# Kernel optimization log

Hardware: AMD Instinct MI355X
Metric: run time of the kernel (lower is better)

## Reference

```python
import jax, jax.numpy as jnp
import numpy as np


def setup_inputs() -> dict:
    key = jax.random.key(0)
    ks = jax.random.split(key, 8)
    B, L, E, U = 32, 2048, 1024, 1024
    s = 0.02
    return {
        "dec_hidden": jax.random.normal(ks[0], (B, E), jnp.float32),
        "enc_output": jax.random.normal(ks[1], (B, L, E), jnp.float32),
        "prev_coverage": jax.random.uniform(ks[2], (B, L, 1), jnp.float32),
        "Ws_k": jax.random.normal(ks[3], (E, U), jnp.float32) * s,
        "Ws_b": jnp.zeros((U,), jnp.float32),
        "Wh_k": jax.random.normal(ks[4], (E, U), jnp.float32) * s,
        "Wh_b": jnp.zeros((U,), jnp.float32),
        "Wc_k": jax.random.normal(ks[5], (1, U), jnp.float32) * s,
        "Wc_b": jnp.zeros((U,), jnp.float32),
        "V_k": jax.random.normal(ks[6], (U, 1), jnp.float32) * s,
        "V_b": jnp.zeros((1,), jnp.float32),
        "enc_pad_mask": jnp.ones((B, L), jnp.int32),
        "use_coverage": 1,
    }


def reference(dec_hidden, enc_output, prev_coverage, Ws_k, Ws_b, Wh_k, Wh_b,
              Wc_k, Wc_b, V_k, V_b, enc_pad_mask, use_coverage):
    # projections: [B,L,U] + [B,1,U] (+ [B,L,U] coverage term)
    pre = jnp.einsum('ble,eu->blu', enc_output, Ws_k) + Ws_b \
        + (dec_hidden @ Wh_k + Wh_b)[:, None, :]
    if use_coverage:
        pre = pre + (prev_coverage @ Wc_k + Wc_b)
    score = jnp.tanh(pre) @ V_k + V_b              # [B, L, 1]
    mask = enc_pad_mask.astype(score.dtype)        # [B, L]
    masked_score = (score[..., 0] * mask)[..., None]  # [B, L, 1]
    attention_weights = jax.nn.softmax(masked_score, axis=1)
    coverage = attention_weights + prev_coverage if use_coverage else attention_weights
    context_vector = jnp.sum(attention_weights * enc_output, axis=1)  # [B, E]
    return (context_vector, attention_weights, coverage)
```

## Files before the change

kernel.cpp:

```cpp
#include <hip/hip_runtime.h>
#include <hip/hip_bf16.h>
#include <math.h>

typedef float f32x4 __attribute__((ext_vector_type(4)));
typedef short short8 __attribute__((ext_vector_type(8)));
typedef unsigned short u16x8 __attribute__((ext_vector_type(8)));

static __device__ __forceinline__ unsigned short f2bf(float f) {
    unsigned u = __builtin_bit_cast(unsigned, f);
    unsigned r = (u + 0x7FFFu + ((u >> 16) & 1u)) >> 16;
    return (unsigned short)r;
}
static __device__ __forceinline__ float bf2f(unsigned short h) {
    unsigned u = ((unsigned)h) << 16;
    return __builtin_bit_cast(float, u);
}
static __device__ __forceinline__ float fast_tanh(float x) {
    float ax = fminf(fmaxf(x, -9.f), 9.f);
    float e = __expf(2.f * ax);
    return 1.f - 2.f / (e + 1.f);
}

#define GLD16(g, l) __builtin_amdgcn_global_load_lds(                        \
    (const __attribute__((address_space(1))) void*)(g),                      \
    (__attribute__((address_space(3))) void*)(l), 16, 0, 0)

__global__ __launch_bounds__(256) void prep_kernel(
    const float* __restrict__ enc, unsigned short* __restrict__ encB,
    const float* __restrict__ ws, unsigned short* __restrict__ wst,
    const float* __restrict__ dh, const float* __restrict__ whk,
    float* __restrict__ base_part)
{
    __shared__ unsigned short tile[64][65];
    __shared__ float dS[128];
    const int bid = blockIdx.x, tid = threadIdx.x;

    if (bid < 16384) {
        const size_t base0 = (size_t)bid * 4096;
#pragma unroll
        for (int i = 0; i < 4; i++) {
            size_t g = base0 + (size_t)i * 1024 + tid * 4;
            f32x4 v = *(const f32x4*)(enc + g);
            ushort4 w;
            w.x = f2bf(v.x); w.y = f2bf(v.y); w.z = f2bf(v.z); w.w = f2bf(v.w);
            *(ushort4*)(encB + g) = w;
        }
    } else if (bid < 16640) {
        const int b2 = bid - 16384;
        const int e0 = (b2 & 15) * 64, u0 = (b2 >> 4) * 64;
#pragma unroll
        for (int i = 0; i < 16; i++) {
            int idx = i * 256 + tid;
            int r = idx >> 6, c = idx & 63;
            tile[r][c] = f2bf(ws[(size_t)(e0 + r) * 1024 + u0 + c]);
        }
        __syncthreads();
#pragma unroll
        for (int i = 0; i < 16; i++) {
            int idx = i * 256 + tid;
            int r = idx >> 6, c = idx & 63;
            wst[(size_t)(u0 + r) * 1024 + e0 + c] = tile[c][r];
        }
    } else {
        const int b3 = bid - 16640;
        const int b = b3 & 31, ec = b3 >> 5;
        const int e0 = ec * 128;
        if (tid < 128) dS[tid] = dh[b * 1024 + e0 + tid];
        __syncthreads();
        f32x4 acc = {0.f, 0.f, 0.f, 0.f};
#pragma unroll 4
        for (int e = 0; e < 128; e++)
            acc += dS[e] * *(const f32x4*)(whk + (size_t)(e0 + e) * 1024 + tid * 4);
        *(f32x4*)(base_part + (size_t)ec * 32768 + b * 1024 + tid * 4) = acc;
    }
}

#define BM 128
#define BN 128
#define BK 32

__global__ __launch_bounds__(256) void score_gemm_fast(
    const unsigned short* __restrict__ encB,
    const unsigned short* __restrict__ wst,
    const float* __restrict__ base_part,
    const float* __restrict__ cov,
    const float* __restrict__ wc,
    const float* __restrict__ vk,
    const float* __restrict__ wsb, const float* __restrict__ whb,
    const float* __restrict__ wcb,
    const int* __restrict__ ucov,
    float* __restrict__ score_part)
{
    __shared__ unsigned short As[2][BM * BK];
    __shared__ unsigned short Bs[2][BN * BK];
    __shared__ float covS[BM];
    __shared__ float baseS[BN], wcS[BN], vvS[BN];
    __shared__ float sred[2][BM];

    const int tid  = threadIdx.x;
    const int row0 = blockIdx.x * BM;
    const int u0   = blockIdx.y * BN;
    const int b    = row0 >> 11;
    const int use_cov = *ucov;

    if (tid < BM) covS[tid] = use_cov ? cov[row0 + tid] : 0.f;
    if (tid < BN) {
        int u = u0 + tid;
        float s = wsb[u] + whb[u] + (use_cov ? wcb[u] : 0.f);
#pragma unroll
        for (int p = 0; p < 8; p++) s += base_part[p * 32768 + b * 1024 + u];
        baseS[tid] = s;
        wcS[tid]   = use_cov ? wc[u] : 0.f;
        vvS[tid]   = vk[u];
    }

    const int lane = tid & 63;
    const int wid  = tid >> 6;
    const int wm   = wid >> 1, wn = wid & 1;
    const int l16  = lane & 15, quad = lane >> 4;

    const int f0 = tid, f1 = 256 + tid;
    const int rA0 = f0 >> 2, rA1 = f1 >> 2;
    const int cA0 = ((f0 & 3) - rA0 - (rA0 >> 2)) & 3;
    const int cA1 = ((f1 & 3) - rA1 - (rA1 >> 2)) & 3;
    const unsigned short* pA0 = encB + (size_t)(row0 + rA0) * 1024 + cA0 * 8;
    const unsigned short* pA1 = encB + (size_t)(row0 + rA1) * 1024 + cA1 * 8;
    const unsigned short* pB0 = wst + (size_t)(u0 + rA0) * 1024 + cA0 * 8;
    const unsigned short* pB1 = wst + (size_t)(u0 + rA1) * 1024 + cA1 * 8;

    int offA[4], offB[4];
#pragma unroll
    for (int t = 0; t < 4; t++) {
        int ra = wm * 64 + t * 16 + l16;
        offA[t] = (ra * 4 + ((quad + ra + (ra >> 2)) & 3)) * 8;
        int rb = wn * 64 + t * 16 + l16;
        offB[t] = (rb * 4 + ((quad + rb + (rb >> 2)) & 3)) * 8;
    }

    f32x4 acc[4][4] = {};

    GLD16(pA0, &As[0][f0 * 8]);
    GLD16(pA1, &As[0][f1 * 8]);
    GLD16(pB0, &Bs[0][f0 * 8]);
    GLD16(pB1, &Bs[0][f1 * 8]);
    pA0 += BK; pA1 += BK; pB0 += BK; pB1 += BK;
    __syncthreads();

    for (int kk = 0; kk < 32; kk++) {
        const int cur = kk & 1, nxt = cur ^ 1;
        if (kk < 31) {
            GLD16(pA0, &As[nxt][f0 * 8]);
            GLD16(pA1, &As[nxt][f1 * 8]);
            GLD16(pB0, &Bs[nxt][f0 * 8]);
            GLD16(pB1, &Bs[nxt][f1 * 8]);
            pA0 += BK; pA1 += BK; pB0 += BK; pB1 += BK;
        }
        short8 a[4], bb[4];
#pragma unroll
        for (int t = 0; t < 4; t++) {
            a[t]  = *(const short8*)&As[cur][offA[t]];
            bb[t] = *(const short8*)&Bs[cur][offB[t]];
        }
#pragma unroll
        for (int i = 0; i < 4; i++)
#pragma unroll
            for (int j = 0; j < 4; j++)
                acc[i][j] = __builtin_amdgcn_mfma_f32_16x16x32_bf16(a[i], bb[j], acc[i][j], 0, 0, 0);
        __syncthreads();
    }

#pragma unroll
    for (int i = 0; i < 4; i++) {
        float part[4] = {0.f, 0.f, 0.f, 0.f};
#pragma unroll
        for (int r = 0; r < 4; r++) {
            int rl = wm * 64 + i * 16 + quad * 4 + r;
            float cv = covS[rl];
#pragma unroll
            for (int j = 0; j < 4; j++) {
                int ul = wn * 64 + j * 16 + l16;
                float pre = acc[i][j][r] + baseS[ul] + cv * wcS[ul];
                part[r] += fast_tanh(pre) * vvS[ul];
            }
        }
#pragma unroll
        for (int r = 0; r < 4; r++) {
            float v = part[r];
            v += __shfl_xor(v, 1);
            v += __shfl_xor(v, 2);
            v += __shfl_xor(v, 4);
            v += __shfl_xor(v, 8);
            if (l16 == 0) sred[wn][wm * 64 + i * 16 + quad * 4 + r] = v;
        }
    }
    __syncthreads();
    if (tid < BM)
        score_part[(size_t)blockIdx.y * 65536 + row0 + tid] = sred[0][tid] + sred[1][tid];
}

__global__ __launch_bounds__(1024) void softmax_kernel(
    const float* __restrict__ score_part, int nplanes,
    const float* __restrict__ vb,
    const int* __restrict__ mask, const float* __restrict__ cov,
    const int* __restrict__ ucov,
    float* __restrict__ attn_out, float* __restrict__ cov_out)
{
    __shared__ float redA[16], redB[16];
    __shared__ float bc0, bc1;
    const int b = blockIdx.x, tid = threadIdx.x;
    const int i0 = b * 2048 + tid, i1 = i0 + 1024;
    const float vbv = vb[0];
    const int uc = *ucov;

    float s0 = 0.f, s1 = 0.f;
    for (int p = 0; p < nplanes; p++) {
        s0 += score_part[(size_t)p * 65536 + i0];
        s1 += score_part[(size_t)p * 65536 + i1];
    }
    s0 = (s0 + vbv) * (float)mask[i0];
    s1 = (s1 + vbv) * (float)mask[i1];

    float m = fmaxf(s0, s1);
#pragma unroll
    for (int off = 1; off < 64; off <<= 1) m = fmaxf(m, __shfl_xor(m, off));
    if ((tid & 63) == 0) redA[tid >> 6] = m;
    __syncthreads();
    if (tid < 16) {
        float v = redA[tid];
#pragma unroll
        for (int off = 1; off < 16; off <<= 1) v = fmaxf(v, __shfl_xor(v, off));
        if (tid == 0) bc0 = v;
    }
    __syncthreads();
    const float M = bc0;

    float e0 = __expf(s0 - M), e1 = __expf(s1 - M);
    float s = e0 + e1;
#pragma unroll
    for (int off = 1; off < 64; off <<= 1) s += __shfl_xor(s, off);
    if ((tid & 63) == 0) redB[tid >> 6] = s;
    __syncthreads();
    if (tid < 16) {
        float v = redB[tid];
#pragma unroll
        for (int off = 1; off < 16; off <<= 1) v += __shfl_xor(v, off);
        if (tid == 0) bc1 = v;
    }
    __syncthreads();
    const float inv = 1.f / bc1;

    float a0 = e0 * inv, a1 = e1 * inv;
    attn_out[i0] = a0;
    attn_out[i1] = a1;
    cov_out[i0] = a0 + (uc ? cov[i0] : 0.f);
    cov_out[i1] = a1 + (uc ? cov[i1] : 0.f);
}

__global__ __launch_bounds__(256) void context_bf16(const unsigned short* __restrict__ encB,
                                                    const float* __restrict__ attn,
                                                    float* __restrict__ out_ctx) {
    __shared__ float aS[2048];
    __shared__ float red[4][64];
    const int b = blockIdx.x, ec = blockIdx.y, tid = threadIdx.x;
    const int e0 = ec * 64;
    for (int i = tid; i < 2048; i += 256) aS[i] = attn[b * 2048 + i];
    __syncthreads();
    const int es = (tid & 7) * 8;
    const int lo = tid >> 3;
    float acc[8] = {};
    for (int l = lo; l < 2048; l += 32) {
        u16x8 w = *(const u16x8*)(encB + (size_t)(b * 2048 + l) * 1024 + e0 + es);
        float a = aS[l];
#pragma unroll
        for (int j = 0; j < 8; j++) acc[j] = fmaf(a, bf2f(w[j]), acc[j]);
    }
#pragma unroll
    for (int j = 0; j < 8; j++) {
        float v = acc[j];
        v += __shfl_xor(v, 8);
        v += __shfl_xor(v, 16);
        v += __shfl_xor(v, 32);
        acc[j] = v;
    }
    const int wv = tid >> 6;
    if ((tid & 63) < 8) {
#pragma unroll
        for (int j = 0; j < 8; j++) red[wv][(tid & 7) * 8 + j] = acc[j];
    }
    __syncthreads();
    if (tid < 64)
        out_ctx[b * 1024 + e0 + tid] = red[0][tid] + red[1][tid] + red[2][tid] + red[3][tid];
}

#define LDT 40
__global__ __launch_bounds__(256) void score_gemm_f32(
    const float* __restrict__ enc, const unsigned short* __restrict__ wst,
    const float* __restrict__ base_part, const float* __restrict__ cov,
    const float* __restrict__ wc, const float* __restrict__ vk,
    const float* __restrict__ wsb, const float* __restrict__ whb,
    const float* __restrict__ wcb,
    const int* __restrict__ ucov, float* __restrict__ score)
{
    __shared__ unsigned short As[BM * LDT];
    __shared__ unsigned short Bs[BN * LDT];
    __shared__ float covS[BM];
    __shared__ float baseS[BN], wcS[BN], vvS[BN];
    const int tid = threadIdx.x;
    const int row0 = blockIdx.x * BM, u0 = blockIdx.y * BN;
    const int b = row0 >> 11;
    const int use_cov = *ucov;
    if (tid < BM) covS[tid] = use_cov ? cov[row0 + tid] : 0.f;
    if (tid < BN) {
        int u = u0 + tid;
        float s = wsb[u] + whb[u] + (use_cov ? wcb[u] : 0.f);
#pragma unroll
        for (int p = 0; p < 8; p++) s += base_part[p * 32768 + b * 1024 + u];
        baseS[tid] = s;
        wcS[tid] = use_cov ? wc[u] : 0.f;
        vvS[tid] = vk[u];
    }
    const int lane = tid & 63, wid = tid >> 6;
    const int wm = wid >> 1, wn = wid & 1;
    const int l16 = lane & 15, quad = lane >> 4;
    f32x4 acc[4][4] = {};
    for (int k0 = 0; k0 < 1024; k0 += BK) {
        __syncthreads();
#pragma unroll
        for (int i = 0; i < 4; i++) {
            int f = i * 256 + tid;
            int r = f >> 3, c4 = f & 7;
            const float* p = enc + (size_t)(row0 + r) * 1024 + k0 + c4 * 4;
            ushort4 w;
            w.x = f2bf(p[0]); w.y = f2bf(p[1]); w.z = f2bf(p[2]); w.w = f2bf(p[3]);
            *(ushort4*)&As[r * LDT + c4 * 4] = w;
        }
#pragma unroll
        for (int i = 0; i < 2; i++) {
            int f = i * 256 + tid;
            int r = f >> 2, c8 = f & 3;
            uint4 w = *(const uint4*)(wst + (size_t)(u0 + r) * 1024 + k0 + c8 * 8);
            *(uint4*)&Bs[r * LDT + c8 * 8] = w;
        }
        __syncthreads();
        short8 a[4], bb[4];
#pragma unroll
        for (int t = 0; t < 4; t++) {
            a[t]  = *(const short8*)&As[(wm * 64 + t * 16 + l16) * LDT + quad * 8];
            bb[t] = *(const short8*)&Bs[(wn * 64 + t * 16 + l16) * LDT + quad * 8];
        }
#pragma unroll
        for (int i = 0; i < 4; i++)
#pragma unroll
            for (int j = 0; j < 4; j++)
                acc[i][j] = __builtin_amdgcn_mfma_f32_16x16x32_bf16(a[i], bb[j], acc[i][j], 0, 0, 0);
    }
#pragma unroll
    for (int i = 0; i < 4; i++) {
        float part[4] = {0.f, 0.f, 0.f, 0.f};
#pragma unroll
        for (int r = 0; r < 4; r++) {
            float cv = covS[wm * 64 + i * 16 + quad * 4 + r];
#pragma unroll
            for (int j = 0; j < 4; j++) {
                int ul = wn * 64 + j * 16 + l16;
                part[r] += fast_tanh(acc[i][j][r] + baseS[ul] + cv * wcS[ul]) * vvS[ul];
            }
        }
#pragma unroll
        for (int r = 0; r < 4; r++) {
            float v = part[r];
            v += __shfl_xor(v, 1);
            v += __shfl_xor(v, 2);
            v += __shfl_xor(v, 4);
            v += __shfl_xor(v, 8);
            if (l16 == 0)
                atomicAdd(&score[row0 + wm * 64 + i * 16 + quad * 4 + r], v);
        }
    }
}

__global__ __launch_bounds__(256) void context_f32(const float* __restrict__ enc,
                                                   const float* __restrict__ attn,
                                                   float* __restrict__ ctx) {
    __shared__ float aS[128];
    const int b = blockIdx.x, lc = blockIdx.y, tid = threadIdx.x;
    const int l0 = lc * 128;
    if (tid < 128) aS[tid] = attn[b * 2048 + l0 + tid];
    __syncthreads();
    const float* p = enc + ((size_t)(b * 2048 + l0)) * 1024 + tid * 4;
    f32x4 acc = {0.f, 0.f, 0.f, 0.f};
#pragma unroll 4
    for (int l = 0; l < 128; l++) acc += *(const f32x4*)(p + (size_t)l * 1024) * aS[l];
    float* o = ctx + b * 1024 + tid * 4;
    atomicAdd(o + 0, acc.x);
    atomicAdd(o + 1, acc.y);
    atomicAdd(o + 2, acc.z);
    atomicAdd(o + 3, acc.w);
}

__global__ __launch_bounds__(256) void prep2_kernel(
    const float* __restrict__ ws, unsigned short* __restrict__ wst,
    const float* __restrict__ dh, const float* __restrict__ whk,
    float* __restrict__ base_part)
{
    __shared__ unsigned short tile[64][65];
    __shared__ float dS[128];
    const int bid = blockIdx.x, tid = threadIdx.x;
    if (bid < 256) {
        const int e0 = (bid & 15) * 64, u0 = (bid >> 4) * 64;
#pragma unroll
        for (int i = 0; i < 16; i++) {
            int idx = i * 256 + tid;
            int r = idx >> 6, c = idx & 63;
            tile[r][c] = f2bf(ws[(size_t)(e0 + r) * 1024 + u0 + c]);
        }
        __syncthreads();
#pragma unroll
        for (int i = 0; i < 16; i++) {
            int idx = i * 256 + tid;
            int r = idx >> 6, c = idx & 63;
            wst[(size_t)(u0 + r) * 1024 + e0 + c] = tile[c][r];
        }
    } else {
        const int b3 = bid - 256;
        const int b = b3 & 31, ec = b3 >> 5;
        const int e0 = ec * 128;
        if (tid < 128) dS[tid] = dh[b * 1024 + e0 + tid];
        __syncthreads();
        f32x4 acc = {0.f, 0.f, 0.f, 0.f};
#pragma unroll 4
        for (int e = 0; e < 128; e++)
            acc += dS[e] * *(const f32x4*)(whk + (size_t)(e0 + e) * 1024 + tid * 4);
        *(f32x4*)(base_part + (size_t)ec * 32768 + b * 1024 + tid * 4) = acc;
    }
}

extern "C" void kernel_launch(void* const* d_in, const int* in_sizes, int n_in,
                              void* d_out, int out_size, void* d_ws, size_t ws_size,
                              hipStream_t stream) {
    const float* dec_hidden = (const float*)d_in[0];
    const float* enc        = (const float*)d_in[1];
    const float* prev_cov   = (const float*)d_in[2];
    const float* Ws_k       = (const float*)d_in[3];
    const float* Ws_b       = (const float*)d_in[4];
    const float* Wh_k       = (const float*)d_in[5];
    const float* Wh_b       = (const float*)d_in[6];
    const float* Wc_k       = (const float*)d_in[7];
    const float* Wc_b       = (const float*)d_in[8];
    const float* V_k        = (const float*)d_in[9];
    const float* V_b        = (const float*)d_in[10];
    const int*   mask       = (const int*)d_in[11];
    const int*   ucov       = (const int*)d_in[12];

    float* out_ctx  = (float*)d_out;
    float* out_attn = out_ctx + 32 * 1024;
    float* out_cov  = out_attn + 65536;

    char* ws = (char*)d_ws;
    unsigned short* wst = (unsigned short*)ws;
    float* base_part  = (float*)(ws + 2097152);
    float* score_part = (float*)(ws + 3145728);
    unsigned short* encB = (unsigned short*)(ws + 5242880);
    const size_t need_fast = 5242880 + (size_t)32 * 2048 * 1024 * 2;

    if (ws_size >= need_fast) {
        prep_kernel<<<16896, 256, 0, stream>>>(enc, encB, Ws_k, wst, dec_hidden, Wh_k, base_part);
        score_gemm_fast<<<dim3(512, 8), 256, 0, stream>>>(
            encB, wst, base_part, prev_cov, Wc_k, V_k, Ws_b, Wh_b, Wc_b, ucov, score_part);
        softmax_kernel<<<32, 1024, 0, stream>>>(score_part, 8, V_b, mask, prev_cov, ucov, out_attn, out_cov);
        context_bf16<<<dim3(32, 16), 256, 0, stream>>>(encB, out_attn, out_ctx);
    } else {
        hipMemsetAsync(score_part, 0, 65536 * sizeof(float), stream);
        hipMemsetAsync(out_ctx, 0, 32 * 1024 * sizeof(float), stream);
        prep2_kernel<<<512, 256, 0, stream>>>(Ws_k, wst, dec_hidden, Wh_k, base_part);
        score_gemm_f32<<<dim3(512, 8), 256, 0, stream>>>(
            enc, wst, base_part, prev_cov, Wc_k, V_k, Ws_b, Wh_b, Wc_b, ucov, score_part);
        softmax_kernel<<<32, 1024, 0, stream>>>(score_part, 1, V_b, mask, prev_cov, ucov, out_attn, out_cov);
        context_f32<<<dim3(32, 16), 256, 0, stream>>>(enc, out_attn, out_ctx);
    }
}
```

Measured before the change: 653.6 us.

## Replace score GEMM with 256x256 eight-phase pipelined MFMA kernel

Rewrites the bf16 score GEMM as 256x256 tiles with 512 threads, a K-step of 64 and an eight-phase schedule. Global-to-LDS loads are interleaved with MFMA groups using explicit barriers, vmcnt waits, sched_barriers and s_setprio. It also XOR-swizzles LDS, remaps blocks for locality, and cuts score partial planes from 8 to 4. The aim is more data reuse per tile and better overlap of memory with compute, at the cost of more registers and LDS, fewer resident blocks, and a fragile hand-tuned schedule.

```diff
diff --git a/kernel.cpp b/kernel.cpp
--- a/kernel.cpp
+++ b/kernel.cpp
@@ -75,11 +75,14 @@
     }
 }
 
-#define BM 128
-#define BN 128
-#define BK 32
-
-__global__ __launch_bounds__(256) void score_gemm_fast(
+#define SBAR()  __builtin_amdgcn_sched_barrier(0)
+#define BARR()  __builtin_amdgcn_s_barrier()
+#define PRIO1() __builtin_amdgcn_s_setprio(1)
+#define PRIO0() __builtin_amdgcn_s_setprio(0)
+#define VMC8()  asm volatile("s_waitcnt vmcnt(8)" ::: "memory")
+#define VMC0()  asm volatile("s_waitcnt vmcnt(0)" ::: "memory")
+
+__global__ __launch_bounds__(512, 2) void score_gemm_8ph(
     const unsigned short* __restrict__ encB,
     const unsigned short* __restrict__ wst,
     const float* __restrict__ base_part,
@@ -91,111 +94,201 @@
     const int* __restrict__ ucov,
     float* __restrict__ score_part)
 {
-    __shared__ unsigned short As[2][BM * BK];
-    __shared__ unsigned short Bs[2][BN * BK];
-    __shared__ float covS[BM];
-    __shared__ float baseS[BN], wcS[BN], vvS[BN];
-    __shared__ float sred[2][BM];
-
-    const int tid  = threadIdx.x;
-    const int row0 = blockIdx.x * BM;
-    const int u0   = blockIdx.y * BN;
-    const int b    = row0 >> 11;
-    const int use_cov = *ucov;
-
-    if (tid < BM) covS[tid] = use_cov ? cov[row0 + tid] : 0.f;
-    if (tid < BN) {
-        int u = u0 + tid;
-        float s = wsb[u] + whb[u] + (use_cov ? wcb[u] : 0.f);
-#pragma unroll
-        for (int p = 0; p < 8; p++) s += base_part[p * 32768 + b * 1024 + u];
-        baseS[tid] = s;
-        wcS[tid]   = use_cov ? wc[u] : 0.f;
-        vvS[tid]   = vk[u];
-    }
+    __shared__ __align__(16) unsigned short As[2][16384];
+    __shared__ __align__(16) unsigned short Bs[2][16384];
+
+    const int tid = threadIdx.x;
+    const int bid = blockIdx.x;
+    const int sidx = bid >> 3;
+    const int row_blk = (bid & 7) * 32 + (sidx >> 2);
+    const int u_blk = sidx & 3;
+    const int row0 = row_blk << 8;
+    const int u0 = u_blk << 8;
 
     const int lane = tid & 63;
     const int wid  = tid >> 6;
-    const int wm   = wid >> 1, wn = wid & 1;
-    const int l16  = lane & 15, quad = lane >> 4;
-
-    const int f0 = tid, f1 = 256 + tid;
-    const int rA0 = f0 >> 2, rA1 = f1 >> 2;
-    const int cA0 = ((f0 & 3) - rA0 - (rA0 >> 2)) & 3;
-    const int cA1 = ((f1 & 3) - rA1 - (rA1 >> 2)) & 3;
-    const unsigned short* pA0 = encB + (size_t)(row0 + rA0) * 1024 + cA0 * 8;
-    const unsigned short* pA1 = encB + (size_t)(row0 + rA1) * 1024 + cA1 * 8;
-    const unsigned short* pB0 = wst + (size_t)(u0 + rA0) * 1024 + cA0 * 8;
-    const unsigned short* pB1 = wst + (size_t)(u0 + rA1) * 1024 + cA1 * 8;
-
-    int offA[4], offB[4];
-#pragma unroll
-    for (int t = 0; t < 4; t++) {
-        int ra = wm * 64 + t * 16 + l16;
-        offA[t] = (ra * 4 + ((quad + ra + (ra >> 2)) & 3)) * 8;
-        int rb = wn * 64 + t * 16 + l16;
-        offB[t] = (rb * 4 + ((quad + rb + (rb >> 2)) & 3)) * 8;
-    }
-
-    f32x4 acc[4][4] = {};
-
-    GLD16(pA0, &As[0][f0 * 8]);
-    GLD16(pA1, &As[0][f1 * 8]);
-    GLD16(pB0, &Bs[0][f0 * 8]);
-    GLD16(pB1, &Bs[0][f1 * 8]);
-    pA0 += BK; pA1 += BK; pB0 += BK; pB1 += BK;
-    __syncthreads();
-
-    for (int kk = 0; kk < 32; kk++) {
-        const int cur = kk & 1, nxt = cur ^ 1;
-        if (kk < 31) {
-            GLD16(pA0, &As[nxt][f0 * 8]);
-            GLD16(pA1, &As[nxt][f1 * 8]);
-            GLD16(pB0, &Bs[nxt][f0 * 8]);
-            GLD16(pB1, &Bs[nxt][f1 * 8]);
-            pA0 += BK; pA1 += BK; pB0 += BK; pB1 += BK;
-        }
-        short8 a[4], bb[4];
-#pragma unroll
-        for (int t = 0; t < 4; t++) {
-            a[t]  = *(const short8*)&As[cur][offA[t]];
-            bb[t] = *(const short8*)&Bs[cur][offB[t]];
-        }
-#pragma unroll
-        for (int i = 0; i < 4; i++)
-#pragma unroll
-            for (int j = 0; j < 4; j++)
-                acc[i][j] = __builtin_amdgcn_mfma_f32_16x16x32_bf16(a[i], bb[j], acc[i][j], 0, 0, 0);
-        __syncthreads();
-    }
-
-#pragma unroll
-    for (int i = 0; i < 4; i++) {
+    const int wm = wid >> 2, wn = wid & 3;
+    const int l16 = lane & 15, quad = lane >> 4;
+
+    const int k8 = (lane & 7) ^ (lane >> 3);
+    unsigned offA[2][2], offB[2][2];
+    int dstA[2][2], dstB[2][2];
+#pragma unroll
+    for (int g = 0; g < 2; g++) {
+        const int uu = wid * 2 + g;
+#pragma unroll
+        for (int h = 0; h < 2; h++) {
+            const int ra = ((uu & 8) << 4) + (h << 6) + ((uu & 7) << 3);
+            const int rb = ((uu >> 2) << 6) + (h << 5) + ((uu & 3) << 3);
+            dstA[g][h] = ra * 64 + lane * 8;
+            dstB[g][h] = rb * 64 + lane * 8;
+            offA[g][h] = (unsigned)(row0 + ra + (lane >> 3)) * 1024u + (unsigned)(k8 * 8);
+            offB[g][h] = (unsigned)(u0 + rb + (lane >> 3)) * 1024u + (unsigned)(k8 * 8);
+        }
+    }
+
+    const int aBase = (wm * 128 + l16) * 64;
+    const int bBase = (wn * 64 + l16) * 64;
+    const int ch0 = ((quad) ^ (l16 & 7)) * 8;
+    const int ch1 = ((4 + quad) ^ (l16 & 7)) * 8;
+
+#define STAGE_A(bf, h, kt) do {                                             \
+    GLD16(encB + offA[0][h] + ((kt) << 6), &As[bf][dstA[0][h]]);            \
+    GLD16(encB + offA[1][h] + ((kt) << 6), &As[bf][dstA[1][h]]); } while (0)
+#define STAGE_B(bf, h, kt) do {                                             \
+    GLD16(wst + offB[0][h] + ((kt) << 6), &Bs[bf][dstB[0][h]]);             \
+    GLD16(wst + offB[1][h] + ((kt) << 6), &Bs[bf][dstB[1][h]]); } while (0)
+
+    f32x4 acc[8][4] = {};
+    short8 aF[4][2], bF0[2][2], bF1[2][2];
+
+#define LOAD_AF(bf, r) do {                                                 \
+    _Pragma("unroll")                                                       \
+    for (int fi = 0; fi < 4; fi++) {                                        \
+        aF[fi][0] = *(const short8*)&As[bf][aBase + (r)*4096 + fi*1024 + ch0]; \
+        aF[fi][1] = *(const short8*)&As[bf][aBase + (r)*4096 + fi*1024 + ch1]; \
+    } } while (0)
+#define LOAD_BF(bf, c, BF) do {                                             \
+    _Pragma("unroll")                                                       \
+    for (int fj = 0; fj < 2; fj++) {                                        \
+        BF[fj][0] = *(const short8*)&Bs[bf][bBase + (c)*2048 + fj*1024 + ch0]; \
+        BF[fj][1] = *(const short8*)&Bs[bf][bBase + (c)*2048 + fj*1024 + ch1]; \
+    } } while (0)
+#define MFMA16(r, c, BF) do {                                               \
+    _Pragma("unroll")                                                       \
+    for (int ks = 0; ks < 2; ks++)                                          \
+    _Pragma("unroll")                                                       \
+    for (int fi = 0; fi < 4; fi++)                                          \
+    _Pragma("unroll")                                                       \
+    for (int fj = 0; fj < 2; fj++)                                          \
+        acc[(r)*4+fi][(c)*2+fj] = __builtin_amdgcn_mfma_f32_16x16x32_bf16(  \
+            aF[fi][ks], BF[fj][ks], acc[(r)*4+fi][(c)*2+fj], 0, 0, 0);      \
+    } while (0)
+
+    STAGE_A(0, 0, 0);
+    STAGE_B(0, 0, 0);
+    STAGE_B(0, 1, 0);
+    STAGE_A(0, 1, 0);
+    STAGE_A(1, 0, 1);
+    STAGE_B(1, 0, 1);
+    STAGE_B(1, 1, 1);
+
+#pragma unroll 1
+    for (int i = 0; i < 7; i++) {
+        const int t1 = 2 * i + 1, t2 = 2 * i + 2, t3 = 2 * i + 3;
+        STAGE_A(1, 1, t1);
+        VMC8();
+        SBAR(); BARR(); SBAR();
+        LOAD_AF(0, 0); LOAD_BF(0, 0, bF0);
+        PRIO1(); MFMA16(0, 0, bF0); PRIO0();
+        SBAR(); BARR(); SBAR();
+        LOAD_BF(0, 1, bF1);
+        STAGE_A(0, 0, t2);
+        SBAR(); BARR(); SBAR();
+        PRIO1(); MFMA16(0, 1, bF1); PRIO0();
+        SBAR(); BARR(); SBAR();
+        LOAD_AF(0, 1);
+        STAGE_B(0, 0, t2);
+        SBAR(); BARR(); SBAR();
+        PRIO1(); MFMA16(1, 0, bF0); PRIO0();
+        SBAR(); BARR(); SBAR();
+        STAGE_B(0, 1, t2);
+        SBAR(); BARR(); SBAR();
+        PRIO1(); MFMA16(1, 1, bF1); PRIO0();
+        SBAR(); BARR(); SBAR();
+        STAGE_A(0, 1, t2);
+        VMC8();
+        SBAR(); BARR(); SBAR();
+        LOAD_AF(1, 0); LOAD_BF(1, 0, bF0);
+        PRIO1(); MFMA16(0, 0, bF0); PRIO0();
+        SBAR(); BARR(); SBAR();
+        LOAD_BF(1, 1, bF1);
+        STAGE_A(1, 0, t3);
+        SBAR(); BARR(); SBAR();
+        PRIO1(); MFMA16(0, 1, bF1); PRIO0();
+        SBAR(); BARR(); SBAR();
+        LOAD_AF(1, 1);
+        STAGE_B(1, 0, t3);
+        SBAR(); BARR(); SBAR();
+        PRIO1(); MFMA16(1, 0, bF0); PRIO0();
+        SBAR(); BARR(); SBAR();
+        STAGE_B(1, 1, t3);
+        SBAR(); BARR(); SBAR();
+        PRIO1(); MFMA16(1, 1, bF1); PRIO0();
+        SBAR(); BARR(); SBAR();
+    }
+
+    STAGE_A(1, 1, 15);
+    VMC8();
+    SBAR(); BARR(); SBAR();
+    LOAD_AF(0, 0); LOAD_BF(0, 0, bF0);
+    PRIO1(); MFMA16(0, 0, bF0); PRIO0();
+    SBAR(); BARR(); SBAR();
+    LOAD_BF(0, 1, bF1);
+    SBAR(); BARR(); SBAR();
+    PRIO1(); MFMA16(0, 1, bF1); PRIO0();
+    SBAR(); BARR(); SBAR();
+    LOAD_AF(0, 1);
+    SBAR(); BARR(); SBAR();
+    PRIO1(); MFMA16(1, 0, bF0); PRIO0();
+    PRIO1(); MFMA16(1, 1, bF1); PRIO0();
+    VMC0();
+    SBAR(); BARR(); SBAR();
+    LOAD_AF(1, 0); LOAD_BF(1, 0, bF0);
+    PRIO1(); MFMA16(0, 0, bF0); PRIO0();
+    LOAD_BF(1, 1, bF1);
+    PRIO1(); MFMA16(0, 1, bF1); PRIO0();
+    LOAD_AF(1, 1);
+    PRIO1(); MFMA16(1, 0, bF0); PRIO0();
+    PRIO1(); MFMA16(1, 1, bF1); PRIO0();
+
+    const int use_cov = *ucov;
+    const int b = row0 >> 11;
+    float baseR[4], wcR[4], vvR[4];
+#pragma unroll
+    for (int cf = 0; cf < 4; cf++) {
+        int u = u0 + wn * 64 + cf * 16 + l16;
+        float s = wsb[u] + whb[u] + (use_cov ? wcb[u] : 0.f);
+#pragma unroll
+        for (int p = 0; p < 8; p++) s += base_part[p * 32768 + b * 1024 + u];
+        baseR[cf] = s;
+        wcR[cf] = use_cov ? wc[u] : 0.f;
+        vvR[cf] = vk[u];
+    }
+    float* sred = (float*)&Bs[0][0];
+#pragma unroll
+    for (int rf = 0; rf < 8; rf++) {
         float part[4] = {0.f, 0.f, 0.f, 0.f};
 #pragma unroll
-        for (int r = 0; r < 4; r++) {
-            int rl = wm * 64 + i * 16 + quad * 4 + r;
-            float cv = covS[rl];
-#pragma unroll
-            for (int j = 0; j < 4; j++) {
-                int ul = wn * 64 + j * 16 + l16;
-                float pre = acc[i][j][r] + baseS[ul] + cv * wcS[ul];
-                part[r] += fast_tanh(pre) * vvS[ul];
+        for (int j = 0; j < 4; j++) {
+            int rl = wm * 128 + rf * 16 + quad * 4 + j;
+            float cvv = use_cov ? cov[row0 + rl] : 0.f;
+#pragma unroll
+            for (int cf = 0; cf < 4; cf++) {
+                float pre = acc[rf][cf][j] + baseR[cf] + cvv * wcR[cf];
+                part[j] += fast_tanh(pre) * vvR[cf];
             }
         }
 #pragma unroll
-        for (int r = 0; r < 4; r++) {
-            float v = part[r];
+        for (int j = 0; j < 4; j++) {
+            float v = part[j];
             v += __shfl_xor(v, 1);
             v += __shfl_xor(v, 2);
             v += __shfl_xor(v, 4);
             v += __shfl_xor(v, 8);
-            if (l16 == 0) sred[wn][wm * 64 + i * 16 + quad * 4 + r] = v;
-        }
-    }
-    __syncthreads();
-    if (tid < BM)
-        score_part[(size_t)blockIdx.y * 65536 + row0 + tid] = sred[0][tid] + sred[1][tid];
+            if (l16 == 0) sred[wn * 256 + wm * 128 + rf * 16 + quad * 4 + j] = v;
+        }
+    }
+    __syncthreads();
+    if (tid < 256)
+        score_part[(size_t)u_blk * 65536 + row0 + tid] =
+            sred[tid] + sred[256 + tid] + sred[512 + tid] + sred[768 + tid];
+
+#undef STAGE_A
+#undef STAGE_B
+#undef LOAD_AF
+#undef LOAD_BF
+#undef MFMA16
 }
 
 __global__ __launch_bounds__(1024) void softmax_kernel(
@@ -292,6 +385,9 @@
         out_ctx[b * 1024 + e0 + tid] = red[0][tid] + red[1][tid] + red[2][tid] + red[3][tid];
 }
 
+#define BM 128
+#define BN 128
+#define BK 32
 #define LDT 40
 __global__ __launch_bounds__(256) void score_gemm_f32(
     const float* __restrict__ enc, const unsigned short* __restrict__ wst,
@@ -465,9 +561,9 @@
 
     if (ws_size >= need_fast) {
         prep_kernel<<<16896, 256, 0, stream>>>(enc, encB, Ws_k, wst, dec_hidden, Wh_k, base_part);
-        score_gemm_fast<<<dim3(512, 8), 256, 0, stream>>>(
+        score_gemm_8ph<<<dim3(1024), dim3(512), 0, stream>>>(
             encB, wst, base_part, prev_cov, Wc_k, V_k, Ws_b, Wh_b, Wc_b, ucov, score_part);
-        softmax_kernel<<<32, 1024, 0, stream>>>(score_part, 8, V_b, mask, prev_cov, ucov, out_attn, out_cov);
+        softmax_kernel<<<32, 1024, 0, stream>>>(score_part, 4, V_b, mask, prev_cov, ucov, out_attn, out_cov);
         context_bf16<<<dim3(32, 16), 256, 0, stream>>>(encB, out_attn, out_ctx);
     } else {
         hipMemsetAsync(score_part, 0, 65536 * sizeof(float), stream);
```

Result: faster. 629.7 us (-3.7%).
